# Performance work log

Hardware: AMD Instinct MI355X
Metric: run time of the kernel (lower is better)

## Reference

```python
import jax, jax.numpy as jnp
import numpy as np

NC = 80
REG_MAX = 16
NO = REG_MAX * 4 + NC  # 144
LEVEL_SHAPES = [(80, 80), (40, 40), (20, 20)]
STRIDES = [8.0, 16.0, 32.0]
CHANNELS = [256, 512, 512]


def _make_anchors():
    """Returns anchor_points (2, A) and stride_tensor (1, A), grid offset 0.5."""
    pts, sts = [], []
    for (h, w), s in zip(LEVEL_SHAPES, STRIDES):
        sx = jnp.arange(w, dtype=jnp.float32) + 0.5
        sy = jnp.arange(h, dtype=jnp.float32) + 0.5
        gy, gx = jnp.meshgrid(sy, sx, indexing='ij')
        pts.append(jnp.stack([gx.ravel(), gy.ravel()], axis=-1))  # (h*w, 2)
        sts.append(jnp.full((h * w,), s, dtype=jnp.float32))
    anchors = jnp.concatenate(pts, axis=0).T          # (2, A)
    strides = jnp.concatenate(sts, axis=0)[None, :]   # (1, A)
    return anchors, strides


def setup_inputs() -> dict:
    key = jax.random.key(0)
    ks = jax.random.split(key, 16)
    inp = {}
    inp['x0'] = jax.random.normal(ks[0], (16, 256, 80, 80), dtype=jnp.float32)
    inp['x1'] = jax.random.normal(ks[1], (16, 512, 40, 40), dtype=jnp.float32)
    inp['x2'] = jax.random.normal(ks[2], (16, 512, 20, 20), dtype=jnp.float32)
    # per-level 1x1 conv head weights: box branch (4*reg_max out), cls branch (nc out)
    for i, c in enumerate(CHANNELS):
        sc = 1.0 / np.sqrt(c)
        inp[f'w_box{i}'] = jax.random.normal(ks[3 + 4 * i], (REG_MAX * 4, c), dtype=jnp.float32) * sc
        inp[f'b_box{i}'] = jax.random.normal(ks[4 + 4 * i], (REG_MAX * 4,), dtype=jnp.float32) * 0.01
        inp[f'w_cls{i}'] = jax.random.normal(ks[5 + 4 * i], (NC, c), dtype=jnp.float32) * sc
        inp[f'b_cls{i}'] = jax.random.normal(ks[6 + 4 * i], (NC,), dtype=jnp.float32) * 0.01
    return inp


def _level_out(x, wb, bb, wc, bc):
    # cat(cv2(x), cv3(x), dim=1) then view(B, no, -1)
    box = jnp.einsum('bchw,oc->bohw', x, wb) + bb[None, :, None, None]
    cls = jnp.einsum('bchw,oc->bohw', x, wc) + bc[None, :, None, None]
    B = x.shape[0]
    return jnp.concatenate([box, cls], axis=1).reshape(B, NO, -1)


def reference(x0, x1, x2,
              w_box0, b_box0, w_cls0, b_cls0,
              w_box1, b_box1, w_cls1, b_cls1,
              w_box2, b_box2, w_cls2, b_cls2):
    xs = [x0, x1, x2]
    wbs = [w_box0, w_box1, w_box2]
    bbs = [b_box0, b_box1, b_box2]
    wcs = [w_cls0, w_cls1, w_cls2]
    bcs = [b_cls0, b_cls1, b_cls2]
    x_cat = jnp.concatenate(
        [_level_out(x, wb, bb, wc, bc) for x, wb, bb, wc, bc in zip(xs, wbs, bbs, wcs, bcs)],
        axis=2)  # (B, 144, A)
    B, _, A = x_cat.shape
    box, cls = x_cat[:, :REG_MAX * 4, :], x_cat[:, REG_MAX * 4:, :]

    # DFL: (B, 4*16, A) -> softmax over 16 bins -> expected distance per side
    p = jax.nn.softmax(box.reshape(B, 4, REG_MAX, A), axis=2)
    dist = jnp.einsum('bkra,r->bka', p, jnp.arange(REG_MAX, dtype=jnp.float32))  # (B, 4, A)

    # dist2bbox (xywh) on anchor grid, scale by stride
    anchors, strides = _make_anchors()
    anc = anchors[None]                 # (1, 2, A)
    lt, rb = dist[:, :2, :], dist[:, 2:, :]
    x1y1 = anc - lt
    x2y2 = anc + rb
    c_xy = (x1y1 + x2y2) * 0.5
    wh = x2y2 - x1y1
    dbox = jnp.concatenate([c_xy, wh], axis=1) * strides[:, None, :]  # (B, 4, A)

    # boxes (B, A, 4), scores (B, A, nc) -- the tensors fed to EfficientNMS_TRT
    boxes = jnp.transpose(dbox, (0, 2, 1))
    scores = jnp.transpose(cls, (0, 2, 1))
    return jnp.concatenate([boxes, scores], axis=-1)  # (B, A, 4 + nc)
```

## Files before the change

kernel.cpp:

```cpp
#include <hip/hip_runtime.h>


typedef __bf16 bf16x8 __attribute__((ext_vector_type(8)));
typedef float  f32x4  __attribute__((ext_vector_type(4)));

#define NTHREADS 256

#define WOFF0 0
#define WOFF1 73728
#define WOFF2 221184
#define WCHUNK_BYTES 18432

__device__ __forceinline__ unsigned int pack_bf16(float a, float b) {
    unsigned int ua = __builtin_bit_cast(unsigned int, a);
    unsigned int ub = __builtin_bit_cast(unsigned int, b);
    return ((ua + 0x8000u) >> 16) | ((ub + 0x8000u) & 0xffff0000u);
}

__device__ __forceinline__ int swz(int row, int kbyte) {
    return row * 128 + (kbyte ^ ((row & 7) << 4));
}

__device__ __forceinline__ void gload_lds16(const void* g, void* l) {
    __builtin_amdgcn_global_load_lds(
        (const __attribute__((address_space(1))) void*)g,
        (__attribute__((address_space(3))) void*)l, 16, 0, 0);
}

__global__ __launch_bounds__(256)
void prep_w_kernel(const float* __restrict__ wb0, const float* __restrict__ wc0,
                   const float* __restrict__ wb1, const float* __restrict__ wc1,
                   const float* __restrict__ wb2, const float* __restrict__ wc2,
                   unsigned char* __restrict__ ws) {
    int uid = blockIdx.x * 256 + threadIdx.x;
    if (uid >= 23040) return;
    const float* wb; const float* wc; int C; size_t off; int uu;
    if (uid < 4608)       { wb = wb0; wc = wc0; C = 256; off = WOFF0; uu = uid; }
    else if (uid < 13824) { wb = wb1; wc = wc1; C = 512; off = WOFF1; uu = uid - 4608; }
    else                  { wb = wb2; wc = wc2; C = 512; off = WOFF2; uu = uid - 13824; }
    const int kunits = C / 8;
    const int row = uu / kunits;
    const int k   = (uu % kunits) * 8;
    const float* src = ((row < 64) ? (wb + row * C) : (wc + (row - 64) * C)) + k;
    const float4 f0 = *(const float4*)(src);
    const float4 f1 = *(const float4*)(src + 4);
    uint4 p;
    p.x = pack_bf16(f0.x, f0.y);
    p.y = pack_bf16(f0.z, f0.w);
    p.z = pack_bf16(f1.x, f1.y);
    p.w = pack_bf16(f1.z, f1.w);
    const int chunk = k >> 6;
    const int kg    = (k & 63) >> 3;
    *(uint4*)(ws + off + (size_t)chunk * WCHUNK_BYTES + swz(row, kg * 16)) = p;
}

template <int LVL>
__device__ __forceinline__ void run_level(
        int rb,
        const float* __restrict__ x,
        const unsigned char* __restrict__ wimg_all,
        const float* __restrict__ bbox, const float* __restrict__ bcls,
        float* __restrict__ out,
        unsigned char* s_w) {

    constexpr int    C      = (LVL == 0) ? 256 : 512;
    constexpr int    GW     = (LVL == 0) ? 80 : (LVL == 1 ? 40 : 20);
    constexpr int    HW     = GW * GW;
    constexpr int    AOFF   = (LVL == 0) ? 0 : (LVL == 1 ? 6400 : 8000);
    constexpr float  STRIDE = (LVL == 0) ? 8.0f : (LVL == 1 ? 16.0f : 32.0f);
    constexpr int    TPB    = (HW + 63) / 64;
    constexpr size_t WOFF   = (LVL == 0) ? WOFF0 : (LVL == 1 ? WOFF1 : WOFF2);
    const int nkc = C / 64;

    const int b    = rb / TPB;
    const int tile = rb % TPB;
    const int hw0  = tile * 64;
    const int nv   = (HW - hw0 < 64) ? (HW - hw0) : 64;

    const int tid  = threadIdx.x;
    const int wv   = tid >> 6;
    const int lane = tid & 63;
    const int col  = lane & 15;
    const int q4   = lane >> 4;

    const float* xb = x + (size_t)b * C * HW;
    const unsigned char* wimg = wimg_all + WOFF;

    const int alocal = wv * 16 + col;
    const int ancc   = (alocal < nv) ? alocal : (nv - 1);
    const float* xanc = xb + hw0 + ancc;

    f32x4 acc[9];
#pragma unroll
    for (int m = 0; m < 9; ++m) acc[m] = (f32x4){0.f, 0.f, 0.f, 0.f};

    float P[16], Q[16];

#define XLOAD(V, CC)                                                        \
    {                                                                       \
        const float* _p = xanc + (size_t)((CC) * 64 + q4 * 8) * HW;         \
        _Pragma("unroll")                                                   \
        for (int _ks = 0; _ks < 2; ++_ks)                                   \
            _Pragma("unroll")                                               \
            for (int _j = 0; _j < 8; ++_j)                                  \
                V[_ks * 8 + _j] = _p[(size_t)(_ks * 32 + _j) * HW];         \
    }

#define WDMA(CC, BUF)                                                       \
    {                                                                       \
        _Pragma("unroll")                                                   \
        for (int _i = 0; _i < 5; ++_i) {                                    \
            int _u = tid + _i * 256;                                        \
            if (_u < 1152)                                                  \
                gload_lds16(wimg + (size_t)(CC) * WCHUNK_BYTES + _u * 16,   \
                            s_w + (BUF) * WCHUNK_BYTES + _u * 16);          \
        }                                                                   \
    }

#define CVT(V, KS, DST)                                                     \
    {                                                                       \
        uint4 _q;                                                           \
        _q.x = pack_bf16(V[(KS) * 8 + 0], V[(KS) * 8 + 1]);                 \
        _q.y = pack_bf16(V[(KS) * 8 + 2], V[(KS) * 8 + 3]);                 \
        _q.z = pack_bf16(V[(KS) * 8 + 4], V[(KS) * 8 + 5]);                 \
        _q.w = pack_bf16(V[(KS) * 8 + 6], V[(KS) * 8 + 7]);                 \
        DST = __builtin_bit_cast(bf16x8, _q);                               \
    }

#define CHUNK_BODY(KC, V, BUF)                                              \
    {                                                                       \
        if ((KC) + 1 < nkc) WDMA((KC) + 1, 1 - (BUF));                      \
        __builtin_amdgcn_sched_barrier(0);                                  \
        bf16x8 _f0, _f1;                                                    \
        CVT(V, 0, _f0);                                                     \
        CVT(V, 1, _f1);                                                     \
        const bool _refill = (KC) + 2 < nkc;                                \
        if (_refill) XLOAD(V, (KC) + 2);                                    \
        __builtin_amdgcn_sched_barrier(0);                                  \
        _Pragma("unroll")                                                   \
        for (int _m = 0; _m < 9; ++_m) {                                    \
            const bf16x8 _a0 = *(const bf16x8*)(s_w + (BUF) * WCHUNK_BYTES  \
                                    + swz(_m * 16 + col, q4 * 16));         \
            acc[_m] = __builtin_amdgcn_mfma_f32_16x16x32_bf16(_a0, _f0,     \
                                                    acc[_m], 0, 0, 0);      \
            const bf16x8 _a1 = *(const bf16x8*)(s_w + (BUF) * WCHUNK_BYTES  \
                                    + swz(_m * 16 + col, 64 + q4 * 16));    \
            acc[_m] = __builtin_amdgcn_mfma_f32_16x16x32_bf16(_a1, _f1,     \
                                                    acc[_m], 0, 0, 0);      \
        }                                                                   \
        __builtin_amdgcn_sched_barrier(0);                                  \
        if (_refill) asm volatile("s_waitcnt vmcnt(16)" ::: "memory");      \
        else         asm volatile("s_waitcnt vmcnt(0)"  ::: "memory");      \
        __builtin_amdgcn_s_barrier();                                       \
        __builtin_amdgcn_sched_barrier(0);                                  \
    }

    WDMA(0, 0);
    __builtin_amdgcn_sched_barrier(0);
    XLOAD(P, 0);
    XLOAD(Q, 1);
    __builtin_amdgcn_sched_barrier(0);
    asm volatile("s_waitcnt vmcnt(32)" ::: "memory");
    __builtin_amdgcn_s_barrier();
    __builtin_amdgcn_sched_barrier(0);

    for (int kc2 = 0; kc2 < nkc; kc2 += 2) {
        CHUNK_BODY(kc2,     P, 0);
        CHUNK_BODY(kc2 + 1, Q, 1);
    }

#undef CHUNK_BODY
#undef CVT
#undef WDMA
#undef XLOAD

    float4 bcv[5];
#pragma unroll
    for (int m = 0; m < 5; ++m)
        bcv[m] = *(const float4*)(bcls + m * 16 + q4 * 4);

    const float LOG2E = 1.44269504088896f;

    const bool valid = alocal < nv;
    const int hw = hw0 + alocal;

    float dist[4];
#pragma unroll
    for (int g = 0; g < 4; ++g) {
        const float4 bbv = *(const float4*)(bbox + g * 16 + q4 * 4);
        const float v0 = acc[g][0] + bbv.x;
        const float v1 = acc[g][1] + bbv.y;
        const float v2 = acc[g][2] + bbv.z;
        const float v3 = acc[g][3] + bbv.w;
        float mx = fmaxf(fmaxf(v0, v1), fmaxf(v2, v3));
        mx = fmaxf(mx, __shfl_xor(mx, 16));
        mx = fmaxf(mx, __shfl_xor(mx, 32));
        const float e0 = __builtin_amdgcn_exp2f((v0 - mx) * LOG2E);
        const float e1 = __builtin_amdgcn_exp2f((v1 - mx) * LOG2E);
        const float e2 = __builtin_amdgcn_exp2f((v2 - mx) * LOG2E);
        const float e3 = __builtin_amdgcn_exp2f((v3 - mx) * LOG2E);
        float s  = e0 + e1 + e2 + e3;
        float ws = e1 + 2.f * e2 + 3.f * e3 + (float)(q4 * 4) * s;
        s  += __shfl_xor(s, 16);
        s  += __shfl_xor(s, 32);
        ws += __shfl_xor(ws, 16);
        ws += __shfl_xor(ws, 32);
        dist[g] = ws / s;
    }

    if (valid) {
        const size_t obase = ((size_t)b * 8400 + AOFF + hw) * 84;
        if (q4 == 0) {
            const float ax = (float)(hw % GW) + 0.5f;
            const float ay = (float)(hw / GW) + 0.5f;
            f32x4 bx;
            bx[0] = (ax + 0.5f * (dist[2] - dist[0])) * STRIDE;
            bx[1] = (ay + 0.5f * (dist[3] - dist[1])) * STRIDE;
            bx[2] = (dist[0] + dist[2]) * STRIDE;
            bx[3] = (dist[1] + dist[3]) * STRIDE;
            *(f32x4*)(out + obase) = bx;
        }
#pragma unroll
        for (int m = 0; m < 5; ++m) {
            f32x4 v;
            v[0] = acc[m + 4][0] + bcv[m].x;
            v[1] = acc[m + 4][1] + bcv[m].y;
            v[2] = acc[m + 4][2] + bcv[m].z;
            v[3] = acc[m + 4][3] + bcv[m].w;
            *(f32x4*)(out + obase + 4 + m * 16 + q4 * 4) = v;
        }
    }
}

__global__ __launch_bounds__(NTHREADS, 4)
void UltralyticsDetect_kernel(
        const float* __restrict__ x0, const float* __restrict__ x1, const float* __restrict__ x2,
        const unsigned char* __restrict__ wimg,
        const float* __restrict__ bb0, const float* __restrict__ bc0,
        const float* __restrict__ bb1, const float* __restrict__ bc1,
        const float* __restrict__ bb2, const float* __restrict__ bc2,
        float* __restrict__ out) {

    __shared__ __align__(16) unsigned char s_w[2 * WCHUNK_BYTES];

    const int bid = blockIdx.x;
    if (bid < 400) {
        run_level<1>(bid, x1, wimg, bb1, bc1, out, s_w);
    } else if (bid < 512) {
        run_level<2>(bid - 400, x2, wimg, bb2, bc2, out, s_w);
    } else {
        run_level<0>(bid - 512, x0, wimg, bb0, bc0, out, s_w);
    }
}

extern "C" void kernel_launch(void* const* d_in, const int* in_sizes, int n_in,
                              void* d_out, int out_size, void* d_ws, size_t ws_size,
                              hipStream_t stream) {
    const float* x0  = (const float*)d_in[0];
    const float* x1  = (const float*)d_in[1];
    const float* x2  = (const float*)d_in[2];
    const float* wb0 = (const float*)d_in[3];
    const float* bb0 = (const float*)d_in[4];
    const float* wc0 = (const float*)d_in[5];
    const float* bc0 = (const float*)d_in[6];
    const float* wb1 = (const float*)d_in[7];
    const float* bb1 = (const float*)d_in[8];
    const float* wc1 = (const float*)d_in[9];
    const float* bc1 = (const float*)d_in[10];
    const float* wb2 = (const float*)d_in[11];
    const float* bb2 = (const float*)d_in[12];
    const float* wc2 = (const float*)d_in[13];
    const float* bc2 = (const float*)d_in[14];

    unsigned char* wimg = (unsigned char*)d_ws;

    prep_w_kernel<<<90, 256, 0, stream>>>(wb0, wc0, wb1, wc1, wb2, wc2, wimg);

    UltralyticsDetect_kernel<<<2112, NTHREADS, 0, stream>>>(
        x0, x1, x2, wimg,
        bb0, bc0, bb1, bc1, bb2, bc2,
        (float*)d_out);
}
```

Before: 50.09 us.

## Double anchor tile per block and halve K chunk to reuse weight fragments

```diff
diff --git a/kernel.cpp b/kernel.cpp
--- a/kernel.cpp
+++ b/kernel.cpp
@@ -6,10 +6,10 @@
 
 #define NTHREADS 256
 
+#define WCHUNK 9216
 #define WOFF0 0
 #define WOFF1 73728
 #define WOFF2 221184
-#define WCHUNK_BYTES 18432
 
 __device__ __forceinline__ unsigned int pack_bf16(float a, float b) {
     unsigned int ua = __builtin_bit_cast(unsigned int, a);
@@ -17,8 +17,8 @@
     return ((ua + 0x8000u) >> 16) | ((ub + 0x8000u) & 0xffff0000u);
 }
 
-__device__ __forceinline__ int swz(int row, int kbyte) {
-    return row * 128 + (kbyte ^ ((row & 7) << 4));
+__device__ __forceinline__ int swz32(int row, int kbyte) {
+    return row * 64 + (kbyte ^ ((((row & 3) ^ ((row >> 2) & 1))) << 4));
 }
 
 __device__ __forceinline__ void gload_lds16(const void* g, void* l) {
@@ -49,9 +49,9 @@
     p.y = pack_bf16(f0.z, f0.w);
     p.z = pack_bf16(f1.x, f1.y);
     p.w = pack_bf16(f1.z, f1.w);
-    const int chunk = k >> 6;
-    const int kg    = (k & 63) >> 3;
-    *(uint4*)(ws + off + (size_t)chunk * WCHUNK_BYTES + swz(row, kg * 16)) = p;
+    const int chunk = k >> 5;
+    const int kg    = (k & 31) >> 3;
+    *(uint4*)(ws + off + (size_t)chunk * WCHUNK + swz32(row, kg * 16)) = p;
 }
 
 template <int LVL>
@@ -68,14 +68,14 @@
     constexpr int    HW     = GW * GW;
     constexpr int    AOFF   = (LVL == 0) ? 0 : (LVL == 1 ? 6400 : 8000);
     constexpr float  STRIDE = (LVL == 0) ? 8.0f : (LVL == 1 ? 16.0f : 32.0f);
-    constexpr int    TPB    = (HW + 63) / 64;
+    constexpr int    TPB    = (HW + 127) / 128;
     constexpr size_t WOFF   = (LVL == 0) ? WOFF0 : (LVL == 1 ? WOFF1 : WOFF2);
-    const int nkc = C / 64;
+    const int nkc = C / 32;
 
     const int b    = rb / TPB;
     const int tile = rb % TPB;
-    const int hw0  = tile * 64;
-    const int nv   = (HW - hw0 < 64) ? (HW - hw0) : 64;
+    const int hw0  = tile * 128;
+    const int nv   = (HW - hw0 < 128) ? (HW - hw0) : 128;
 
     const int tid  = threadIdx.x;
     const int wv   = tid >> 6;
@@ -86,90 +86,89 @@
     const float* xb = x + (size_t)b * C * HW;
     const unsigned char* wimg = wimg_all + WOFF;
 
-    const int alocal = wv * 16 + col;
-    const int ancc   = (alocal < nv) ? alocal : (nv - 1);
-    const float* xanc = xb + hw0 + ancc;
-
-    f32x4 acc[9];
-#pragma unroll
-    for (int m = 0; m < 9; ++m) acc[m] = (f32x4){0.f, 0.f, 0.f, 0.f};
-
-    float P[16], Q[16];
-
-#define XLOAD(V, CC)                                                        \
+    const int a0 = wv * 16 + col;
+    const int a1 = 64 + a0;
+    const int a0c = (a0 < nv) ? a0 : (nv - 1);
+    const int a1c = (a1 < nv) ? a1 : (nv - 1);
+    const float* xanc0 = xb + hw0 + a0c;
+    const float* xanc1 = xb + hw0 + a1c;
+
+    f32x4 acc[9][2];
+#pragma unroll
+    for (int m = 0; m < 9; ++m) {
+        acc[m][0] = (f32x4){0.f, 0.f, 0.f, 0.f};
+        acc[m][1] = (f32x4){0.f, 0.f, 0.f, 0.f};
+    }
+
+    float P[16];
+
+#define XLOAD(CC)                                                           \
     {                                                                       \
-        const float* _p = xanc + (size_t)((CC) * 64 + q4 * 8) * HW;         \
+        const size_t _kb = (size_t)((CC) * 32 + q4 * 8) * HW;               \
+        const float* _p0 = xanc0 + _kb;                                     \
+        const float* _p1 = xanc1 + _kb;                                     \
         _Pragma("unroll")                                                   \
-        for (int _ks = 0; _ks < 2; ++_ks)                                   \
-            _Pragma("unroll")                                               \
-            for (int _j = 0; _j < 8; ++_j)                                  \
-                V[_ks * 8 + _j] = _p[(size_t)(_ks * 32 + _j) * HW];         \
+        for (int _j = 0; _j < 8; ++_j) {                                    \
+            P[_j]     = _p0[(size_t)_j * HW];                               \
+            P[8 + _j] = _p1[(size_t)_j * HW];                               \
+        }                                                                   \
     }
 
 #define WDMA(CC, BUF)                                                       \
     {                                                                       \
         _Pragma("unroll")                                                   \
-        for (int _i = 0; _i < 5; ++_i) {                                    \
+        for (int _i = 0; _i < 3; ++_i) {                                    \
             int _u = tid + _i * 256;                                        \
-            if (_u < 1152)                                                  \
-                gload_lds16(wimg + (size_t)(CC) * WCHUNK_BYTES + _u * 16,   \
-                            s_w + (BUF) * WCHUNK_BYTES + _u * 16);          \
+            if (_u < 576)                                                   \
+                gload_lds16(wimg + (size_t)(CC) * WCHUNK + _u * 16,         \
+                            s_w + (BUF) * WCHUNK + _u * 16);                \
         }                                                                   \
     }
 
-#define CVT(V, KS, DST)                                                     \
+#define CVT(O, DST)                                                         \
     {                                                                       \
         uint4 _q;                                                           \
-        _q.x = pack_bf16(V[(KS) * 8 + 0], V[(KS) * 8 + 1]);                 \
-        _q.y = pack_bf16(V[(KS) * 8 + 2], V[(KS) * 8 + 3]);                 \
-        _q.z = pack_bf16(V[(KS) * 8 + 4], V[(KS) * 8 + 5]);                 \
-        _q.w = pack_bf16(V[(KS) * 8 + 6], V[(KS) * 8 + 7]);                 \
+        _q.x = pack_bf16(P[(O) + 0], P[(O) + 1]);                           \
+        _q.y = pack_bf16(P[(O) + 2], P[(O) + 3]);                           \
+        _q.z = pack_bf16(P[(O) + 4], P[(O) + 5]);                           \
+        _q.w = pack_bf16(P[(O) + 6], P[(O) + 7]);                           \
         DST = __builtin_bit_cast(bf16x8, _q);                               \
     }
 
-#define CHUNK_BODY(KC, V, BUF)                                              \
-    {                                                                       \
-        if ((KC) + 1 < nkc) WDMA((KC) + 1, 1 - (BUF));                      \
-        __builtin_amdgcn_sched_barrier(0);                                  \
-        bf16x8 _f0, _f1;                                                    \
-        CVT(V, 0, _f0);                                                     \
-        CVT(V, 1, _f1);                                                     \
-        const bool _refill = (KC) + 2 < nkc;                                \
-        if (_refill) XLOAD(V, (KC) + 2);                                    \
-        __builtin_amdgcn_sched_barrier(0);                                  \
-        _Pragma("unroll")                                                   \
-        for (int _m = 0; _m < 9; ++_m) {                                    \
-            const bf16x8 _a0 = *(const bf16x8*)(s_w + (BUF) * WCHUNK_BYTES  \
-                                    + swz(_m * 16 + col, q4 * 16));         \
-            acc[_m] = __builtin_amdgcn_mfma_f32_16x16x32_bf16(_a0, _f0,     \
-                                                    acc[_m], 0, 0, 0);      \
-            const bf16x8 _a1 = *(const bf16x8*)(s_w + (BUF) * WCHUNK_BYTES  \
-                                    + swz(_m * 16 + col, 64 + q4 * 16));    \
-            acc[_m] = __builtin_amdgcn_mfma_f32_16x16x32_bf16(_a1, _f1,     \
-                                                    acc[_m], 0, 0, 0);      \
-        }                                                                   \
-        __builtin_amdgcn_sched_barrier(0);                                  \
-        if (_refill) asm volatile("s_waitcnt vmcnt(16)" ::: "memory");      \
-        else         asm volatile("s_waitcnt vmcnt(0)"  ::: "memory");      \
-        __builtin_amdgcn_s_barrier();                                       \
-        __builtin_amdgcn_sched_barrier(0);                                  \
-    }
-
     WDMA(0, 0);
+    XLOAD(0);
     __builtin_amdgcn_sched_barrier(0);
-    XLOAD(P, 0);
-    XLOAD(Q, 1);
-    __builtin_amdgcn_sched_barrier(0);
-    asm volatile("s_waitcnt vmcnt(32)" ::: "memory");
+    asm volatile("s_waitcnt vmcnt(16)" ::: "memory");
     __builtin_amdgcn_s_barrier();
     __builtin_amdgcn_sched_barrier(0);
 
-    for (int kc2 = 0; kc2 < nkc; kc2 += 2) {
-        CHUNK_BODY(kc2,     P, 0);
-        CHUNK_BODY(kc2 + 1, Q, 1);
-    }
-
-#undef CHUNK_BODY
+    for (int kc = 0; kc < nkc; ++kc) {
+        const unsigned char* wb = s_w + (kc & 1) * WCHUNK;
+        const bool more = (kc + 1 < nkc);
+
+        if (more) WDMA(kc + 1, (kc & 1) ^ 1);
+
+        bf16x8 fA, fB;
+        CVT(0, fA);
+        CVT(8, fB);
+
+        if (more) XLOAD(kc + 1);
+        __builtin_amdgcn_sched_barrier(0);
+
+#pragma unroll
+        for (int m = 0; m < 9; ++m) {
+            const bf16x8 af = *(const bf16x8*)(wb + swz32(m * 16 + col, q4 * 16));
+            acc[m][0] = __builtin_amdgcn_mfma_f32_16x16x32_bf16(af, fA, acc[m][0], 0, 0, 0);
+            acc[m][1] = __builtin_amdgcn_mfma_f32_16x16x32_bf16(af, fB, acc[m][1], 0, 0, 0);
+        }
+        __builtin_amdgcn_sched_barrier(0);
+
+        if (more) asm volatile("s_waitcnt vmcnt(16)" ::: "memory");
+        else      asm volatile("s_waitcnt vmcnt(0)"  ::: "memory");
+        __builtin_amdgcn_s_barrier();
+        __builtin_amdgcn_sched_barrier(0);
+    }
+
 #undef CVT
 #undef WDMA
 #undef XLOAD
@@ -181,53 +180,57 @@
 
     const float LOG2E = 1.44269504088896f;
 
-    const bool valid = alocal < nv;
-    const int hw = hw0 + alocal;
-
-    float dist[4];
-#pragma unroll
-    for (int g = 0; g < 4; ++g) {
-        const float4 bbv = *(const float4*)(bbox + g * 16 + q4 * 4);
-        const float v0 = acc[g][0] + bbv.x;
-        const float v1 = acc[g][1] + bbv.y;
-        const float v2 = acc[g][2] + bbv.z;
-        const float v3 = acc[g][3] + bbv.w;
-        float mx = fmaxf(fmaxf(v0, v1), fmaxf(v2, v3));
-        mx = fmaxf(mx, __shfl_xor(mx, 16));
-        mx = fmaxf(mx, __shfl_xor(mx, 32));
-        const float e0 = __builtin_amdgcn_exp2f((v0 - mx) * LOG2E);
-        const float e1 = __builtin_amdgcn_exp2f((v1 - mx) * LOG2E);
-        const float e2 = __builtin_amdgcn_exp2f((v2 - mx) * LOG2E);
-        const float e3 = __builtin_amdgcn_exp2f((v3 - mx) * LOG2E);
-        float s  = e0 + e1 + e2 + e3;
-        float ws = e1 + 2.f * e2 + 3.f * e3 + (float)(q4 * 4) * s;
-        s  += __shfl_xor(s, 16);
-        s  += __shfl_xor(s, 32);
-        ws += __shfl_xor(ws, 16);
-        ws += __shfl_xor(ws, 32);
-        dist[g] = ws / s;
-    }
-
-    if (valid) {
-        const size_t obase = ((size_t)b * 8400 + AOFF + hw) * 84;
-        if (q4 == 0) {
-            const float ax = (float)(hw % GW) + 0.5f;
-            const float ay = (float)(hw / GW) + 0.5f;
-            f32x4 bx;
-            bx[0] = (ax + 0.5f * (dist[2] - dist[0])) * STRIDE;
-            bx[1] = (ay + 0.5f * (dist[3] - dist[1])) * STRIDE;
-            bx[2] = (dist[0] + dist[2]) * STRIDE;
-            bx[3] = (dist[1] + dist[3]) * STRIDE;
-            *(f32x4*)(out + obase) = bx;
+#pragma unroll
+    for (int nf = 0; nf < 2; ++nf) {
+        const int alocal = nf * 64 + wv * 16 + col;
+        const bool valid = alocal < nv;
+        const int hw = hw0 + alocal;
+
+        float dist[4];
+#pragma unroll
+        for (int g = 0; g < 4; ++g) {
+            const float4 bbv = *(const float4*)(bbox + g * 16 + q4 * 4);
+            const float v0 = acc[g][nf][0] + bbv.x;
+            const float v1 = acc[g][nf][1] + bbv.y;
+            const float v2 = acc[g][nf][2] + bbv.z;
+            const float v3 = acc[g][nf][3] + bbv.w;
+            float mx = fmaxf(fmaxf(v0, v1), fmaxf(v2, v3));
+            mx = fmaxf(mx, __shfl_xor(mx, 16));
+            mx = fmaxf(mx, __shfl_xor(mx, 32));
+            const float e0 = __builtin_amdgcn_exp2f((v0 - mx) * LOG2E);
+            const float e1 = __builtin_amdgcn_exp2f((v1 - mx) * LOG2E);
+            const float e2 = __builtin_amdgcn_exp2f((v2 - mx) * LOG2E);
+            const float e3 = __builtin_amdgcn_exp2f((v3 - mx) * LOG2E);
+            float s  = e0 + e1 + e2 + e3;
+            float ws = e1 + 2.f * e2 + 3.f * e3 + (float)(q4 * 4) * s;
+            s  += __shfl_xor(s, 16);
+            s  += __shfl_xor(s, 32);
+            ws += __shfl_xor(ws, 16);
+            ws += __shfl_xor(ws, 32);
+            dist[g] = ws / s;
         }
-#pragma unroll
-        for (int m = 0; m < 5; ++m) {
-            f32x4 v;
-            v[0] = acc[m + 4][0] + bcv[m].x;
-            v[1] = acc[m + 4][1] + bcv[m].y;
-            v[2] = acc[m + 4][2] + bcv[m].z;
-            v[3] = acc[m + 4][3] + bcv[m].w;
-            *(f32x4*)(out + obase + 4 + m * 16 + q4 * 4) = v;
+
+        if (valid) {
+            const size_t obase = ((size_t)b * 8400 + AOFF + hw) * 84;
+            if (q4 == 0) {
+                const float ax = (float)(hw % GW) + 0.5f;
+                const float ay = (float)(hw / GW) + 0.5f;
+                f32x4 bx;
+                bx[0] = (ax + 0.5f * (dist[2] - dist[0])) * STRIDE;
+                bx[1] = (ay + 0.5f * (dist[3] - dist[1])) * STRIDE;
+                bx[2] = (dist[0] + dist[2]) * STRIDE;
+                bx[3] = (dist[1] + dist[3]) * STRIDE;
+                *(f32x4*)(out + obase) = bx;
+            }
+#pragma unroll
+            for (int m = 0; m < 5; ++m) {
+                f32x4 v;
+                v[0] = acc[m + 4][nf][0] + bcv[m].x;
+                v[1] = acc[m + 4][nf][1] + bcv[m].y;
+                v[2] = acc[m + 4][nf][2] + bcv[m].z;
+                v[3] = acc[m + 4][nf][3] + bcv[m].w;
+                *(f32x4*)(out + obase + 4 + m * 16 + q4 * 4) = v;
+            }
         }
     }
 }
@@ -241,15 +244,15 @@
         const float* __restrict__ bb2, const float* __restrict__ bc2,
         float* __restrict__ out) {
 
-    __shared__ __align__(16) unsigned char s_w[2 * WCHUNK_BYTES];
+    __shared__ __align__(16) unsigned char s_w[2 * WCHUNK];
 
     const int bid = blockIdx.x;
-    if (bid < 400) {
+    if (bid < 208) {
         run_level<1>(bid, x1, wimg, bb1, bc1, out, s_w);
-    } else if (bid < 512) {
-        run_level<2>(bid - 400, x2, wimg, bb2, bc2, out, s_w);
+    } else if (bid < 272) {
+        run_level<2>(bid - 208, x2, wimg, bb2, bc2, out, s_w);
     } else {
-        run_level<0>(bid - 512, x0, wimg, bb0, bc0, out, s_w);
+        run_level<0>(bid - 272, x0, wimg, bb0, bc0, out, s_w);
     }
 }
 
@@ -276,7 +279,7 @@
 
     prep_w_kernel<<<90, 256, 0, stream>>>(wb0, wc0, wb1, wc1, wb2, wc2, wimg);
 
-    UltralyticsDetect_kernel<<<2112, NTHREADS, 0, stream>>>(
+    UltralyticsDetect_kernel<<<1072, NTHREADS, 0, stream>>>(
         x0, x1, x2, wimg,
         bb0, bc0, bb1, bc1, bb2, bc2,
         (float*)d_out);
```

Result: slower. 51.11 us (+2.0%).
